# Optimization experiments

Hardware: AMD Instinct MI355X
Metric: run time of the kernel (lower is better)

Reference implementation:

```python
import jax, jax.numpy as jnp
import numpy as np

HIDDEN = 4096
NUM_HEADS = 32
HEAD_DIM = HIDDEN // NUM_HEADS  # 128
ROPE_THETA = 10000.0
B, S = 1, 2048


def setup_inputs() -> dict:
    key = jax.random.key(0)
    k1, k2, k3, k4 = jax.random.split(key, 4)
    positions = jnp.broadcast_to(jnp.arange(S, dtype=jnp.int32), (B, S))
    hidden_states = jax.random.normal(k1, (B, S, HIDDEN), dtype=jnp.float32)
    # fused QKV projection (bias=True), output projection (bias=False)
    w_qkv = jax.random.normal(k2, (HIDDEN, 3 * HIDDEN), dtype=jnp.float32) * (HIDDEN ** -0.5)
    b_qkv = jax.random.normal(k3, (3 * HIDDEN,), dtype=jnp.float32) * 0.01
    w_o = jax.random.normal(k4, (HIDDEN, HIDDEN), dtype=jnp.float32) * (HIDDEN ** -0.5)
    return {"positions": positions, "hidden_states": hidden_states,
            "w_qkv": w_qkv, "b_qkv": b_qkv, "w_o": w_o}


def _apply_rope(x, positions):
    # x: [B, S, N, D]; NeoX-style rotate-half RoPE, rotary_dim == head_dim
    half = HEAD_DIM // 2
    inv_freq = 1.0 / (ROPE_THETA ** (jnp.arange(0, half, dtype=jnp.float32) / half))
    angles = positions.astype(jnp.float32)[..., None] * inv_freq  # [B, S, half]
    cos = jnp.cos(angles)[:, :, None, :]  # [B, S, 1, half]
    sin = jnp.sin(angles)[:, :, None, :]
    x1, x2 = x[..., :half], x[..., half:]
    return jnp.concatenate([x1 * cos - x2 * sin, x2 * cos + x1 * sin], axis=-1)


def reference(positions, hidden_states, w_qkv, b_qkv, w_o):
    qkv = jnp.einsum('bsh,hd->bsd', hidden_states, w_qkv) + b_qkv  # [B, S, 3H]
    q, k, v = jnp.split(qkv, 3, axis=-1)
    q = q.reshape(B, S, NUM_HEADS, HEAD_DIM)
    k = k.reshape(B, S, NUM_HEADS, HEAD_DIM)
    v = v.reshape(B, S, NUM_HEADS, HEAD_DIM)
    q = _apply_rope(q, positions)
    k = _apply_rope(k, positions)
    scale = HEAD_DIM ** -0.5
    scores = jnp.einsum('bqnd,bknd->bnqk', q, k) * scale  # [B, N, S, S]
    causal = jnp.tril(jnp.ones((S, S), dtype=bool))
    scores = jnp.where(causal, scores, jnp.finfo(scores.dtype).min)
    probs = jax.nn.softmax(scores, axis=-1)
    attn = jnp.einsum('bnqk,bknd->bqnd', probs, v).reshape(B, S, HIDDEN)
    return jnp.einsum('bsh,ho->bso', attn, w_o)
```

## Files before the change

### kernel.cpp

```cpp
#include <hip/hip_runtime.h>
#include <hip/hip_bf16.h>

#define S_LEN 2048
#define HID   4096
#define NH    32
#define HD    128
#define KD    4096

typedef __attribute__((ext_vector_type(4))) float f32x4;
typedef __attribute__((ext_vector_type(8))) short s16x8;
typedef __attribute__((ext_vector_type(4))) short s16x4;

#define AS1 __attribute__((address_space(1)))
#define AS3 __attribute__((address_space(3)))

__device__ __forceinline__ void gl_lds16(const void* g, void* l) {
  __builtin_amdgcn_global_load_lds((const AS1 void*)g, (AS3 void*)l, 16, 0, 0);
}

__device__ inline short f2bf(float f) {
  union { float f; unsigned u; } v; v.f = f;
  return (short)((v.u + 0x7fffu + ((v.u >> 16) & 1u)) >> 16);
}
__device__ inline float bf2f(short s) {
  union { unsigned u; float f; } v; v.u = ((unsigned)(unsigned short)s) << 16;
  return v.f;
}
__device__ inline unsigned packbf(float a, float b) {
  return (unsigned)(unsigned short)f2bf(a) | ((unsigned)(unsigned short)f2bf(b) << 16);
}

__global__ __launch_bounds__(256)
void cvt_kernel(const float* __restrict__ A, short* __restrict__ Ab) {
  const size_t i = ((size_t)blockIdx.x * 256 + threadIdx.x) * 8;
  f32x4 v0 = *(const f32x4*)&A[i];
  f32x4 v1 = *(const f32x4*)&A[i + 4];
  s16x8 r;
  r[0]=f2bf(v0[0]); r[1]=f2bf(v0[1]); r[2]=f2bf(v0[2]); r[3]=f2bf(v0[3]);
  r[4]=f2bf(v1[0]); r[5]=f2bf(v1[1]); r[6]=f2bf(v1[2]); r[7]=f2bf(v1[3]);
  *(s16x8*)&Ab[i] = r;
}

__global__ __launch_bounds__(256)
void transcvt_kernel(const float* __restrict__ W, short* __restrict__ Wt, const int N) {
  __shared__ float tile[64][65];
  const int k0 = blockIdx.x * 64, n0 = blockIdx.y * 64;
  const int t = threadIdx.x;
#pragma unroll
  for (int i = 0; i < 16; ++i) {
    const int e = i * 256 + t;
    const int k = e >> 6, n = e & 63;
    tile[n][k] = W[(size_t)(k0 + k) * N + n0 + n];
  }
  __syncthreads();
  const int nn = t >> 2, ks = (t & 3) * 16;
  s16x8 a, b;
#pragma unroll
  for (int i = 0; i < 8; i++) a[i] = f2bf(tile[nn][ks + i]);
#pragma unroll
  for (int i = 0; i < 8; i++) b[i] = f2bf(tile[nn][ks + 8 + i]);
  *(s16x8*)&Wt[(size_t)(n0 + nn) * KD + k0 + ks]     = a;
  *(s16x8*)&Wt[(size_t)(n0 + nn) * KD + k0 + ks + 8] = b;
}

template<int EPI>
__global__ __launch_bounds__(256, 2)
void gemm5_kernel(const short* __restrict__ A, const short* __restrict__ Bt,
                  const float* __restrict__ bias,
                  short* __restrict__ Qb, short* __restrict__ Kb, short* __restrict__ Vb,
                  float* __restrict__ Cout)
{
  __shared__ char sm[3][24576] __attribute__((aligned(128)));
  const int KD2 = KD * 2;
  const int bid = blockIdx.x;
  const int xcd = bid & 7, idx = bid >> 3;
  const int m0 = (idx & 7) * 256;
  const int n0 = (xcd * ((EPI == 0) ? 12 : 4) + (idx >> 3)) * 128;

  const int t = threadIdx.x, lane = t & 63, c = lane & 15, g = lane >> 4;
  const int w = t >> 6, wr = w >> 1, wc = w & 1;
  const int flip = ((c >> 1) & 7) << 4;
  const int laneA = wr * 8192 + ((c * 64 + g * 16) ^ flip);
  const int laneB = 16384 + wc * 4096 + ((c * 64 + g * 16) ^ flip);

  const char* srcA[4];
  const char* srcB[2];
#pragma unroll
  for (int j = 0; j < 4; ++j) {
    const int la = j * 4096 + t * 16;
    const int ls = la ^ ((la >> 3) & 0x70);
    srcA[j] = (const char*)A + (size_t)(m0 + (ls >> 6)) * KD2 + (ls & 63);
  }
#pragma unroll
  for (int j = 0; j < 2; ++j) {
    const int la = j * 4096 + t * 16;
    const int ls = la ^ ((la >> 3) & 0x70);
    srcB[j] = (const char*)Bt + (size_t)(n0 + (ls >> 6)) * KD2 + (ls & 63);
  }

  f32x4 acc[8][4];
#pragma unroll
  for (int i = 0; i < 8; i++)
#pragma unroll
    for (int j = 0; j < 4; j++) acc[i][j] = (f32x4){0.f, 0.f, 0.f, 0.f};

#define STG(S, H) do {                                        \
    const size_t ko_ = (size_t)(H) * 64;                      \
    gl_lds16(srcA[0] + ko_, sm[S] + t * 16);                  \
    gl_lds16(srcA[1] + ko_, sm[S] + 4096  + t * 16);          \
    gl_lds16(srcA[2] + ko_, sm[S] + 8192  + t * 16);          \
    gl_lds16(srcA[3] + ko_, sm[S] + 12288 + t * 16);          \
    gl_lds16(srcB[0] + ko_, sm[S] + 16384 + t * 16);          \
    gl_lds16(srcB[1] + ko_, sm[S] + 20480 + t * 16);          \
  } while (0)

#define COMP(S) do {                                                       \
    const char* b_ = sm[S];                                                \
    s16x8 a_[8], bb_[4];                                                   \
    _Pragma("unroll")                                                      \
    for (int mi = 0; mi < 8; ++mi) a_[mi] = *(const s16x8*)(b_ + laneA + mi * 1024); \
    _Pragma("unroll")                                                      \
    for (int ni = 0; ni < 4; ++ni) bb_[ni] = *(const s16x8*)(b_ + laneB + ni * 1024); \
    __builtin_amdgcn_s_setprio(1);                                         \
    _Pragma("unroll")                                                      \
    for (int mi = 0; mi < 8; ++mi)                                         \
      _Pragma("unroll")                                                    \
      for (int ni = 0; ni < 4; ++ni)                                       \
        acc[mi][ni] = __builtin_amdgcn_mfma_f32_16x16x32_bf16(a_[mi], bb_[ni], acc[mi][ni], 0, 0, 0); \
    __builtin_amdgcn_s_setprio(0);                                         \
  } while (0)

#define WAIT6 asm volatile("s_waitcnt vmcnt(6)" ::: "memory")
#define WAIT0 asm volatile("s_waitcnt vmcnt(0)" ::: "memory")
#define BARR  do { __builtin_amdgcn_s_barrier(); asm volatile("" ::: "memory"); } while (0)

  STG(0, 0); STG(1, 1);
  for (int j = 0; j < 42; ++j) {
    const int h = 3 * j;
    WAIT6; BARR; STG(2, h + 2); COMP(0);
    WAIT6; BARR; STG(0, h + 3); COMP(1);
    WAIT6; BARR; STG(1, h + 4); COMP(2);
  }
  WAIT6; BARR; COMP(0);
  WAIT0; BARR; COMP(1);

#undef STG
#undef COMP
#undef WAIT6
#undef WAIT0
#undef BARR

  if (EPI == 0) {
#pragma unroll
    for (int ni = 0; ni < 4; ++ni) {
      const int ncol = n0 + wc * 64 + ni * 16 + c;
      const int which = ncol >> 12;
      const int h = (ncol >> 7) & 31;
      const int dcl = ncol & 127;
      short* dst = (which == 0) ? Qb : ((which == 1) ? Kb : Vb);
      const float bv = bias[ncol];
#pragma unroll
      for (int mi = 0; mi < 8; ++mi)
#pragma unroll
        for (int jj = 0; jj < 4; ++jj) {
          const int row = m0 + wr * 128 + mi * 16 + g * 4 + jj;
          dst[((size_t)h * S_LEN + row) * HD + dcl] = f2bf(acc[mi][ni][jj] + bv);
        }
    }
  } else {
#pragma unroll
    for (int ni = 0; ni < 4; ++ni) {
      const int ncol = n0 + wc * 64 + ni * 16 + c;
#pragma unroll
      for (int mi = 0; mi < 8; ++mi)
#pragma unroll
        for (int jj = 0; jj < 4; ++jj) {
          const int row = m0 + wr * 128 + mi * 16 + g * 4 + jj;
          Cout[(size_t)row * HID + ncol] = acc[mi][ni][jj];
        }
    }
  }
}

__global__ __launch_bounds__(256, 3)
void gemm7_kernel(const short* __restrict__ A, const short* __restrict__ Bt,
                  float* __restrict__ Cout)
{
  __shared__ char sm[3][16384] __attribute__((aligned(128)));
  const int KD2 = KD * 2;
  const int bid = blockIdx.x;
  const int xcd = bid & 7, idx = bid >> 3;
  const int m0 = (idx & 15) * 128;
  const int n0 = (xcd * 4 + (idx >> 4)) * 128;

  const int t = threadIdx.x, lane = t & 63, c = lane & 15, g = lane >> 4;
  const int w = t >> 6, wr = w >> 1, wc = w & 1;
  const int flip = ((c >> 1) & 7) << 4;
  const int laneA = wr * 4096 + ((c * 64 + g * 16) ^ flip);
  const int laneB = 8192 + wc * 4096 + ((c * 64 + g * 16) ^ flip);

  const char* srcA[2];
  const char* srcB[2];
#pragma unroll
  for (int j = 0; j < 2; ++j) {
    const int la = j * 4096 + t * 16;
    const int ls = la ^ ((la >> 3) & 0x70);
    srcA[j] = (const char*)A  + (size_t)(m0 + (ls >> 6)) * KD2 + (ls & 63);
    srcB[j] = (const char*)Bt + (size_t)(n0 + (ls >> 6)) * KD2 + (ls & 63);
  }

  f32x4 acc[4][4];
#pragma unroll
  for (int i = 0; i < 4; i++)
#pragma unroll
    for (int j = 0; j < 4; j++) acc[i][j] = (f32x4){0.f, 0.f, 0.f, 0.f};

#define STG7(S, H) do {                                       \
    const size_t ko_ = (size_t)(H) * 64;                      \
    gl_lds16(srcA[0] + ko_, sm[S] + t * 16);                  \
    gl_lds16(srcA[1] + ko_, sm[S] + 4096  + t * 16);          \
    gl_lds16(srcB[0] + ko_, sm[S] + 8192  + t * 16);          \
    gl_lds16(srcB[1] + ko_, sm[S] + 12288 + t * 16);          \
  } while (0)

#define COMP7(S) do {                                                      \
    const char* b_ = sm[S];                                                \
    s16x8 a_[4], bb_[4];                                                   \
    _Pragma("unroll")                                                      \
    for (int mi = 0; mi < 4; ++mi) a_[mi] = *(const s16x8*)(b_ + laneA + mi * 1024); \
    _Pragma("unroll")                                                      \
    for (int ni = 0; ni < 4; ++ni) bb_[ni] = *(const s16x8*)(b_ + laneB + ni * 1024); \
    __builtin_amdgcn_s_setprio(1);                                         \
    _Pragma("unroll")                                                      \
    for (int mi = 0; mi < 4; ++mi)                                         \
      _Pragma("unroll")                                                    \
      for (int ni = 0; ni < 4; ++ni)                                       \
        acc[mi][ni] = __builtin_amdgcn_mfma_f32_16x16x32_bf16(a_[mi], bb_[ni], acc[mi][ni], 0, 0, 0); \
    __builtin_amdgcn_s_setprio(0);                                         \
  } while (0)

#define WAIT4 asm volatile("s_waitcnt vmcnt(4)" ::: "memory")
#define WAIT0 asm volatile("s_waitcnt vmcnt(0)" ::: "memory")
#define BARR  do { __builtin_amdgcn_s_barrier(); asm volatile("" ::: "memory"); } while (0)

  STG7(0, 0); STG7(1, 1);
  for (int j = 0; j < 42; ++j) {
    const int h = 3 * j;
    WAIT4; BARR; STG7(2, h + 2); COMP7(0);
    WAIT4; BARR; STG7(0, h + 3); COMP7(1);
    WAIT4; BARR; STG7(1, h + 4); COMP7(2);
  }
  WAIT4; BARR; COMP7(0);
  WAIT0; BARR; COMP7(1);

#undef STG7
#undef COMP7
#undef WAIT4
#undef WAIT0
#undef BARR

#pragma unroll
  for (int ni = 0; ni < 4; ++ni) {
    const int ncol = n0 + wc * 64 + ni * 16 + c;
#pragma unroll
    for (int mi = 0; mi < 4; ++mi)
#pragma unroll
      for (int jj = 0; jj < 4; ++jj) {
        const int row = m0 + wr * 64 + mi * 16 + g * 4 + jj;
        Cout[(size_t)row * HID + ncol] = acc[mi][ni][jj];
      }
  }
}

template<int EPI, int ABF16>
__global__ __launch_bounds__(256)
void gemm_kernel(const void* __restrict__ Av, const float* __restrict__ B,
                 const float* __restrict__ bias, const int N,
                 short* __restrict__ Qb, short* __restrict__ Kb, short* __restrict__ Vb,
                 float* __restrict__ Cout)
{
  __shared__ short As[128][40];
  __shared__ short Bs[128][40];
  const int m0 = blockIdx.x * 128;
  const int nb = blockIdx.y * 128;
  const int t  = threadIdx.x;
  const int w = t >> 6, lane = t & 63, c = lane & 15, g = lane >> 4;
  const int wm = (w >> 1) * 64, wn = (w & 1) * 64;

  f32x4 acc[4][4];
#pragma unroll
  for (int i = 0; i < 4; i++)
#pragma unroll
    for (int j = 0; j < 4; j++) acc[i][j] = (f32x4){0.f, 0.f, 0.f, 0.f};

  const int ar = t >> 3;
  const int ac = (t & 7) * 4;
  const int bn = t & 127;
  const int bkq = (t >> 7) * 16;

  for (int k0 = 0; k0 < KD; k0 += 32) {
#pragma unroll
    for (int rr = 0; rr < 4; rr++) {
      const int row = rr * 32 + ar;
      if (ABF16) {
        *(s16x4*)&As[row][ac] =
          *(const s16x4*)((const short*)Av + (size_t)(m0 + row) * KD + k0 + ac);
      } else {
        f32x4 v = *(const f32x4*)((const float*)Av + (size_t)(m0 + row) * KD + k0 + ac);
        s16x4 pk;
        pk[0] = f2bf(v[0]); pk[1] = f2bf(v[1]); pk[2] = f2bf(v[2]); pk[3] = f2bf(v[3]);
        *(s16x4*)&As[row][ac] = pk;
      }
    }
    const float* pB = B + (size_t)(k0 + bkq) * N + nb + bn;
    s16x8 b0, b1;
#pragma unroll
    for (int i = 0; i < 8; i++) b0[i] = f2bf(pB[(size_t)i * N]);
#pragma unroll
    for (int i = 0; i < 8; i++) b1[i] = f2bf(pB[(size_t)(i + 8) * N]);
    *(s16x8*)&Bs[bn][bkq]     = b0;
    *(s16x8*)&Bs[bn][bkq + 8] = b1;
    __syncthreads();
    s16x8 af[4], bfr[4];
#pragma unroll
    for (int i = 0; i < 4; i++) af[i]  = *(const s16x8*)&As[wm + i * 16 + c][g * 8];
#pragma unroll
    for (int i = 0; i < 4; i++) bfr[i] = *(const s16x8*)&Bs[wn + i * 16 + c][g * 8];
#pragma unroll
    for (int mi = 0; mi < 4; mi++)
#pragma unroll
      for (int ni = 0; ni < 4; ni++)
        acc[mi][ni] = __builtin_amdgcn_mfma_f32_16x16x32_bf16(af[mi], bfr[ni], acc[mi][ni], 0, 0, 0);
    __syncthreads();
  }

  if (EPI == 0) {
    const int which = nb >> 12;
    const int h = (nb & 4095) >> 7;
    short* dst = (which == 0) ? Qb : ((which == 1) ? Kb : Vb);
#pragma unroll
    for (int ni = 0; ni < 4; ni++) {
      const int d = wn + ni * 16 + c;
      const float bv = bias[nb + d];
#pragma unroll
      for (int mi = 0; mi < 4; mi++)
#pragma unroll
        for (int j = 0; j < 4; j++) {
          const int row = m0 + wm + mi * 16 + g * 4 + j;
          dst[((size_t)h * S_LEN + row) * HD + d] = f2bf(acc[mi][ni][j] + bv);
        }
    }
  } else {
#pragma unroll
    for (int ni = 0; ni < 4; ni++) {
      const int n = nb + wn + ni * 16 + c;
#pragma unroll
      for (int mi = 0; mi < 4; mi++)
#pragma unroll
        for (int j = 0; j < 4; j++) {
          const int row = m0 + wm + mi * 16 + g * 4 + j;
          Cout[(size_t)row * N + n] = acc[mi][ni][j];
        }
    }
  }
}

__global__ void rope_kernel(const int* __restrict__ positions,
                            short* __restrict__ Qb, short* __restrict__ Kb)
{
  const int s = blockIdx.x;
  const int h = blockIdx.y * 4 + threadIdx.y;
  const int d = threadIdx.x;
  const float pos = (float)positions[s];
  const float inv_freq = exp2f(-(float)d * 0.20762050593046014f);
  const float ang = pos * inv_freq;
  float sn, cs;
  sincosf(ang, &sn, &cs);
  const size_t base = ((size_t)h * S_LEN + s) * HD + d;
  const float scale = 0.08838834764831845f;
  float x1 = bf2f(Qb[base]), x2 = bf2f(Qb[base + 64]);
  Qb[base]      = f2bf((x1 * cs - x2 * sn) * scale);
  Qb[base + 64] = f2bf((x2 * cs + x1 * sn) * scale);
  x1 = bf2f(Kb[base]); x2 = bf2f(Kb[base + 64]);
  Kb[base]      = f2bf(x1 * cs - x2 * sn);
  Kb[base + 64] = f2bf(x2 * cs + x1 * sn);
}

__global__ __launch_bounds__(256)
void vtrans_kernel(const short* __restrict__ V, short* __restrict__ Vt)
{
  __shared__ short tile[64][72];
  const int h = blockIdx.z;
  const int s0 = blockIdx.x * 64;
  const int d0 = blockIdx.y * 64;
  const int tx = threadIdx.x & 63, ty = threadIdx.x >> 6;
  for (int r = ty; r < 64; r += 4)
    tile[r][tx] = V[((size_t)h * S_LEN + s0 + r) * HD + d0 + tx];
  __syncthreads();
  for (int r = ty; r < 64; r += 4)
    Vt[((size_t)h * HD + d0 + r) * S_LEN + s0 + tx] = tile[tx][r];
}

__global__ __launch_bounds__(512)
void attn_kernel(const short* __restrict__ Q, const short* __restrict__ Kg,
                 const short* __restrict__ Vtg, short* __restrict__ attn_out)
{
  __shared__ short Ks[2][64][128];
  __shared__ short Vs[2][128][72];
  const int h = blockIdx.y;
  const int q0 = blockIdx.x * 128;
  const int t = threadIdx.x;
  const int w = t >> 6, lane = t & 63, c = lane & 15, g = lane >> 4;
  const short* Qh = Q   + (size_t)h * S_LEN * HD;
  const short* Kh = Kg  + (size_t)h * S_LEN * HD;
  const short* Vh = Vtg + (size_t)h * HD * S_LEN;

  const int krow = t >> 4, kch = t & 15;
  const int vrow = t >> 3, vch = t & 7;
  const int ksw = (kch ^ ((krow & 3) | ((krow >> 1) & 4))) * 16;

  const int rbase = (c >> 2) * 8 + (c & 3);
  const int sb = (rbase & 3) | ((rbase >> 1) & 4);
  int koff[4];
#pragma unroll
  for (int di = 0; di < 4; ++di) koff[di] = ((di * 4 + g) ^ sb) * 16;

  const int qg = q0 + w * 16 + c;
  s16x8 qf[4];
#pragma unroll
  for (int di = 0; di < 4; di++)
    qf[di] = *(const s16x8*)&Qh[(size_t)qg * HD + di * 32 + g * 8];

  f32x4 o[8];
#pragma unroll
  for (int dt = 0; dt < 8; dt++) o[dt] = (f32x4){0.f, 0.f, 0.f, 0.f};
  float m_r = -3.0e38f, l_r = 0.f;

  const int nt = q0 / 64 + 2;

  {
#pragma unroll
    for (int i = 0; i < 2; ++i) {
      s16x8 gK = *(const s16x8*)&Kh[(size_t)(i * 32 + krow) * HD + kch * 8];
      s16x8 gV = *(const s16x8*)&Vh[(size_t)(i * 64 + vrow) * S_LEN + vch * 8];
      *(s16x8*)((char*)&Ks[0][0][0] + (i * 32 + krow) * 256 + ksw) = gK;
      *(s16x8*)&Vs[0][i * 64 + vrow][vch * 8] = gV;
    }
  }
  __syncthreads();

  for (int kt = 0; kt < nt; kt++) {
    const int cur = kt & 1;
    const int kb = kt * 64;
    s16x8 gK0, gK1, gV0, gV1;
    if (kt + 1 < nt) {
      gK0 = *(const s16x8*)&Kh[(size_t)(kb + 64 + krow) * HD + kch * 8];
      gK1 = *(const s16x8*)&Kh[(size_t)(kb + 96 + krow) * HD + kch * 8];
      gV0 = *(const s16x8*)&Vh[(size_t)vrow * S_LEN + kb + 64 + vch * 8];
      gV1 = *(const s16x8*)&Vh[(size_t)(64 + vrow) * S_LEN + kb + 64 + vch * 8];
    }
    f32x4 sA = (f32x4){0,0,0,0}, sB = (f32x4){0,0,0,0};
    f32x4 sC = (f32x4){0,0,0,0}, sD = (f32x4){0,0,0,0};
    const char* kb_ = (const char*)&Ks[cur][0][0] + rbase * 256;
#pragma unroll
    for (int di = 0; di < 4; ++di) {
      const char* p = kb_ + koff[di];
      s16x8 kA = *(const s16x8*)(p);
      s16x8 kB = *(const s16x8*)(p + 1024);
      s16x8 kC = *(const s16x8*)(p + 8192);
      s16x8 kD = *(const s16x8*)(p + 9216);
      sA = __builtin_amdgcn_mfma_f32_16x16x32_bf16(kA, qf[di], sA, 0, 0, 0);
      sB = __builtin_amdgcn_mfma_f32_16x16x32_bf16(kB, qf[di], sB, 0, 0, 0);
      sC = __builtin_amdgcn_mfma_f32_16x16x32_bf16(kC, qf[di], sC, 0, 0, 0);
      sD = __builtin_amdgcn_mfma_f32_16x16x32_bf16(kD, qf[di], sD, 0, 0, 0);
    }
    float v[16];
#pragma unroll
    for (int j = 0; j < 4; ++j) {
      v[j]      = (kb + 8 * g + j      <= qg) ? sA[j] : -__builtin_inff();
      v[4 + j]  = (kb + 8 * g + 4 + j  <= qg) ? sB[j] : -__builtin_inff();
      v[8 + j]  = (kb + 32 + 8 * g + j     <= qg) ? sC[j] : -__builtin_inff();
      v[12 + j] = (kb + 32 + 8 * g + 4 + j <= qg) ? sD[j] : -__builtin_inff();
    }
    float mx = v[0];
#pragma unroll
    for (int i = 1; i < 16; ++i) mx = fmaxf(mx, v[i]);
    mx = fmaxf(mx, __shfl_xor(mx, 16, 64));
    mx = fmaxf(mx, __shfl_xor(mx, 32, 64));
    const float mn = fmaxf(m_r, mx);
    if (!__all(mn - m_r <= 8.0f)) {
      const float al = __expf(m_r - mn);
      l_r *= al;
#pragma unroll
      for (int dt = 0; dt < 8; dt++)
#pragma unroll
        for (int j = 0; j < 4; j++) o[dt][j] *= al;
      m_r = mn;
    }
    float p[16];
    float rs = 0.f;
#pragma unroll
    for (int i = 0; i < 16; ++i) { p[i] = __expf(v[i] - m_r); rs += p[i]; }
    rs += __shfl_xor(rs, 16, 64);
    rs += __shfl_xor(rs, 32, 64);
    l_r += rs;
    union { s16x8 v8; unsigned u[4]; } pb0, pb1;
    pb0.u[0] = packbf(p[0], p[1]);   pb0.u[1] = packbf(p[2], p[3]);
    pb0.u[2] = packbf(p[4], p[5]);   pb0.u[3] = packbf(p[6], p[7]);
    pb1.u[0] = packbf(p[8], p[9]);   pb1.u[1] = packbf(p[10], p[11]);
    pb1.u[2] = packbf(p[12], p[13]); pb1.u[3] = packbf(p[14], p[15]);
#pragma unroll
    for (int dt = 0; dt < 8; dt++) {
      s16x8 vf0 = *(const s16x8*)&Vs[cur][dt * 16 + c][g * 8];
      s16x8 vf1 = *(const s16x8*)&Vs[cur][dt * 16 + c][32 + g * 8];
      o[dt] = __builtin_amdgcn_mfma_f32_16x16x32_bf16(vf0, pb0.v8, o[dt], 0, 0, 0);
      o[dt] = __builtin_amdgcn_mfma_f32_16x16x32_bf16(vf1, pb1.v8, o[dt], 0, 0, 0);
    }
    __syncthreads();
    if (kt + 1 < nt) {
      *(s16x8*)((char*)&Ks[cur ^ 1][0][0] + krow * 256 + ksw)        = gK0;
      *(s16x8*)((char*)&Ks[cur ^ 1][0][0] + (32 + krow) * 256 + ksw) = gK1;
      *(s16x8*)&Vs[cur ^ 1][vrow][vch * 8]      = gV0;
      *(s16x8*)&Vs[cur ^ 1][64 + vrow][vch * 8] = gV1;
    }
    __syncthreads();
  }

  const float inv_l = 1.0f / l_r;
#pragma unroll
  for (int dt = 0; dt < 8; dt++) {
    s16x4 pk;
#pragma unroll
    for (int j = 0; j < 4; j++) pk[j] = f2bf(o[dt][j] * inv_l);
    *(s16x4*)&attn_out[(size_t)qg * HID + h * HD + dt * 16 + g * 4] = pk;
  }
}

extern "C" void kernel_launch(void* const* d_in, const int* in_sizes, int n_in,
                              void* d_out, int out_size, void* d_ws, size_t ws_size,
                              hipStream_t stream)
{
  const int*   positions = (const int*)d_in[0];
  const float* hidden    = (const float*)d_in[1];
  const float* w_qkv     = (const float*)d_in[2];
  const float* b_qkv     = (const float*)d_in[3];
  const float* w_o       = (const float*)d_in[4];
  float* out = (float*)d_out;

  char* ws = (char*)d_ws;
  const size_t MB = (size_t)1 << 20;

  if (ws_size >= 224 * MB) {
    short* Ah    = (short*)(ws);
    short* Wqt   = (short*)(ws + 16 * MB);
    short* Wot   = (short*)(ws + 112 * MB);
    short* Qb    = (short*)(ws + 144 * MB);
    short* Kb    = (short*)(ws + 160 * MB);
    short* Vb    = (short*)(ws + 176 * MB);
    short* Vt    = (short*)(ws + 192 * MB);
    short* attnb = (short*)(ws + 208 * MB);

    cvt_kernel<<<4096, 256, 0, stream>>>(hidden, Ah);
    transcvt_kernel<<<dim3(KD / 64, 3 * HID / 64), 256, 0, stream>>>(w_qkv, Wqt, 3 * HID);
    transcvt_kernel<<<dim3(KD / 64, HID / 64), 256, 0, stream>>>(w_o, Wot, HID);
    gemm5_kernel<0><<<768, 256, 0, stream>>>(Ah, Wqt, b_qkv, Qb, Kb, Vb, nullptr);
    rope_kernel<<<dim3(S_LEN, NH / 4), dim3(64, 4), 0, stream>>>(positions, Qb, Kb);
    vtrans_kernel<<<dim3(S_LEN / 64, HD / 64, NH), 256, 0, stream>>>(Vb, Vt);
    attn_kernel<<<dim3(S_LEN / 128, NH), 512, 0, stream>>>(Qb, Kb, Vt, attnb);
    gemm7_kernel<<<512, 256, 0, stream>>>(attnb, Wot, out);
  } else {
    short* Qb    = (short*)(ws);
    short* Kb    = (short*)(ws + 16 * MB);
    short* Vb    = (short*)(ws + 32 * MB);
    short* Vt    = (short*)(ws + 48 * MB);
    short* attnb = (short*)(ws + 64 * MB);

    gemm_kernel<0, 0><<<dim3(16, 96), 256, 0, stream>>>(hidden, w_qkv, b_qkv, 3 * HID,
                                                        Qb, Kb, Vb, nullptr);
    rope_kernel<<<dim3(S_LEN, NH / 4), dim3(64, 4), 0, stream>>>(positions, Qb, Kb);
    vtrans_kernel<<<dim3(S_LEN / 64, HD / 64, NH), 256, 0, stream>>>(Vb, Vt);
    attn_kernel<<<dim3(S_LEN / 128, NH), 512, 0, stream>>>(Qb, Kb, Vt, attnb);
    gemm_kernel<1, 1><<<dim3(16, 32), 256, 0, stream>>>(attnb, w_o, nullptr, HID,
                                                        nullptr, nullptr, nullptr, out);
  }
}
```

Before: 495.5 us.

## Pair mirrored causal query tiles per attention block to balance work and share K/V loads

Each attention block now handles two 128-row query tiles, ib and 15-ib, so every block streams the same total number of K/V tiles, and the K/V tiles loaded into LDS are shared by both query tiles. The grid is halved to 8x32 blocks. The change also skips causal masking on fully visible tiles and raises wave priority around the MFMA sections. In exchange, register pressure roughly doubles (two sets of accumulators and Q fragments), which may spill or lower occupancy, and only 256 blocks remain to fill the GPU.

```diff
diff --git a/kernel.cpp b/kernel.cpp
--- a/kernel.cpp
+++ b/kernel.cpp
@@ -408,7 +408,11 @@
   __shared__ short Ks[2][64][128];
   __shared__ short Vs[2][128][72];
   const int h = blockIdx.y;
-  const int q0 = blockIdx.x * 128;
+  const int ib = blockIdx.x;
+  const int q0a = ib * 128;
+  const int q0b = (15 - ib) * 128;
+  const int nt0 = 2 * ib + 2;
+  const int nt1 = 32 - 2 * ib;
   const int t = threadIdx.x;
   const int w = t >> 6, lane = t & 63, c = lane & 15, g = lane >> 4;
   const short* Qh = Q   + (size_t)h * S_LEN * HD;
@@ -425,18 +429,67 @@
 #pragma unroll
   for (int di = 0; di < 4; ++di) koff[di] = ((di * 4 + g) ^ sb) * 16;
 
-  const int qg = q0 + w * 16 + c;
-  s16x8 qf[4];
-#pragma unroll
-  for (int di = 0; di < 4; di++)
-    qf[di] = *(const s16x8*)&Qh[(size_t)qg * HD + di * 32 + g * 8];
-
-  f32x4 o[8];
-#pragma unroll
-  for (int dt = 0; dt < 8; dt++) o[dt] = (f32x4){0.f, 0.f, 0.f, 0.f};
-  float m_r = -3.0e38f, l_r = 0.f;
-
-  const int nt = q0 / 64 + 2;
+  const int qga = q0a + w * 16 + c;
+  const int qgb = q0b + w * 16 + c;
+  s16x8 qfa[4], qfb[4];
+#pragma unroll
+  for (int di = 0; di < 4; di++) {
+    qfa[di] = *(const s16x8*)&Qh[(size_t)qga * HD + di * 32 + g * 8];
+    qfb[di] = *(const s16x8*)&Qh[(size_t)qgb * HD + di * 32 + g * 8];
+  }
+
+  f32x4 oa[8], ob[8];
+#pragma unroll
+  for (int dt = 0; dt < 8; dt++) {
+    oa[dt] = (f32x4){0.f, 0.f, 0.f, 0.f};
+    ob[dt] = (f32x4){0.f, 0.f, 0.f, 0.f};
+  }
+  float m_a = -3.0e38f, l_a = 0.f, m_b = -3.0e38f, l_b = 0.f;
+
+#define SM_PANEL(SA, SB, SC, SD, QG, FULL, MR, LR, OARR, PB0, PB1) do {        \
+    float v_[16];                                                              \
+    if (FULL) {                                                                \
+      _Pragma("unroll")                                                        \
+      for (int j = 0; j < 4; ++j) {                                            \
+        v_[j] = SA[j]; v_[4 + j] = SB[j]; v_[8 + j] = SC[j]; v_[12 + j] = SD[j]; \
+      }                                                                        \
+    } else {                                                                   \
+      _Pragma("unroll")                                                        \
+      for (int j = 0; j < 4; ++j) {                                            \
+        v_[j]      = (kb + 8 * g + j          <= (QG)) ? SA[j] : -__builtin_inff(); \
+        v_[4 + j]  = (kb + 8 * g + 4 + j      <= (QG)) ? SB[j] : -__builtin_inff(); \
+        v_[8 + j]  = (kb + 32 + 8 * g + j     <= (QG)) ? SC[j] : -__builtin_inff(); \
+        v_[12 + j] = (kb + 32 + 8 * g + 4 + j <= (QG)) ? SD[j] : -__builtin_inff(); \
+      }                                                                        \
+    }                                                                          \
+    float mx_ = v_[0];                                                         \
+    _Pragma("unroll")                                                          \
+    for (int ii = 1; ii < 16; ++ii) mx_ = fmaxf(mx_, v_[ii]);                  \
+    mx_ = fmaxf(mx_, __shfl_xor(mx_, 16, 64));                                 \
+    mx_ = fmaxf(mx_, __shfl_xor(mx_, 32, 64));                                 \
+    const float mn_ = fmaxf(MR, mx_);                                          \
+    if (!__all(mn_ - MR <= 8.0f)) {                                            \
+      const float al_ = __expf(MR - mn_);                                      \
+      LR *= al_;                                                               \
+      _Pragma("unroll")                                                        \
+      for (int dt = 0; dt < 8; ++dt)                                           \
+        _Pragma("unroll")                                                      \
+        for (int j = 0; j < 4; ++j) OARR[dt][j] *= al_;                        \
+      MR = mn_;                                                                \
+    }                                                                          \
+    float p_[16], rs_ = 0.f;                                                   \
+    _Pragma("unroll")                                                          \
+    for (int ii = 0; ii < 16; ++ii) { p_[ii] = __expf(v_[ii] - MR); rs_ += p_[ii]; } \
+    rs_ += __shfl_xor(rs_, 16, 64);                                            \
+    rs_ += __shfl_xor(rs_, 32, 64);                                            \
+    LR += rs_;                                                                 \
+    union { s16x8 v8; unsigned u[4]; } pu0_, pu1_;                             \
+    pu0_.u[0] = packbf(p_[0], p_[1]);   pu0_.u[1] = packbf(p_[2], p_[3]);      \
+    pu0_.u[2] = packbf(p_[4], p_[5]);   pu0_.u[3] = packbf(p_[6], p_[7]);      \
+    pu1_.u[0] = packbf(p_[8], p_[9]);   pu1_.u[1] = packbf(p_[10], p_[11]);    \
+    pu1_.u[2] = packbf(p_[12], p_[13]); pu1_.u[3] = packbf(p_[14], p_[15]);    \
+    PB0 = pu0_.v8; PB1 = pu1_.v8;                                              \
+  } while (0)
 
   {
 #pragma unroll
@@ -449,75 +502,85 @@
   }
   __syncthreads();
 
-  for (int kt = 0; kt < nt; kt++) {
+  for (int kt = 0; kt < nt1; kt++) {
     const int cur = kt & 1;
     const int kb = kt * 64;
+    const bool do0 = (kt < nt0);
     s16x8 gK0, gK1, gV0, gV1;
-    if (kt + 1 < nt) {
+    if (kt + 1 < nt1) {
       gK0 = *(const s16x8*)&Kh[(size_t)(kb + 64 + krow) * HD + kch * 8];
       gK1 = *(const s16x8*)&Kh[(size_t)(kb + 96 + krow) * HD + kch * 8];
       gV0 = *(const s16x8*)&Vh[(size_t)vrow * S_LEN + kb + 64 + vch * 8];
       gV1 = *(const s16x8*)&Vh[(size_t)(64 + vrow) * S_LEN + kb + 64 + vch * 8];
     }
-    f32x4 sA = (f32x4){0,0,0,0}, sB = (f32x4){0,0,0,0};
-    f32x4 sC = (f32x4){0,0,0,0}, sD = (f32x4){0,0,0,0};
-    const char* kb_ = (const char*)&Ks[cur][0][0] + rbase * 256;
-#pragma unroll
-    for (int di = 0; di < 4; ++di) {
-      const char* p = kb_ + koff[di];
-      s16x8 kA = *(const s16x8*)(p);
-      s16x8 kB = *(const s16x8*)(p + 1024);
-      s16x8 kC = *(const s16x8*)(p + 8192);
-      s16x8 kD = *(const s16x8*)(p + 9216);
-      sA = __builtin_amdgcn_mfma_f32_16x16x32_bf16(kA, qf[di], sA, 0, 0, 0);
-      sB = __builtin_amdgcn_mfma_f32_16x16x32_bf16(kB, qf[di], sB, 0, 0, 0);
-      sC = __builtin_amdgcn_mfma_f32_16x16x32_bf16(kC, qf[di], sC, 0, 0, 0);
-      sD = __builtin_amdgcn_mfma_f32_16x16x32_bf16(kD, qf[di], sD, 0, 0, 0);
-    }
-    float v[16];
-#pragma unroll
-    for (int j = 0; j < 4; ++j) {
-      v[j]      = (kb + 8 * g + j      <= qg) ? sA[j] : -__builtin_inff();
-      v[4 + j]  = (kb + 8 * g + 4 + j  <= qg) ? sB[j] : -__builtin_inff();
-      v[8 + j]  = (kb + 32 + 8 * g + j     <= qg) ? sC[j] : -__builtin_inff();
-      v[12 + j] = (kb + 32 + 8 * g + 4 + j <= qg) ? sD[j] : -__builtin_inff();
-    }
-    float mx = v[0];
-#pragma unroll
-    for (int i = 1; i < 16; ++i) mx = fmaxf(mx, v[i]);
-    mx = fmaxf(mx, __shfl_xor(mx, 16, 64));
-    mx = fmaxf(mx, __shfl_xor(mx, 32, 64));
-    const float mn = fmaxf(m_r, mx);
-    if (!__all(mn - m_r <= 8.0f)) {
-      const float al = __expf(m_r - mn);
-      l_r *= al;
-#pragma unroll
-      for (int dt = 0; dt < 8; dt++)
-#pragma unroll
-        for (int j = 0; j < 4; j++) o[dt][j] *= al;
-      m_r = mn;
-    }
-    float p[16];
-    float rs = 0.f;
-#pragma unroll
-    for (int i = 0; i < 16; ++i) { p[i] = __expf(v[i] - m_r); rs += p[i]; }
-    rs += __shfl_xor(rs, 16, 64);
-    rs += __shfl_xor(rs, 32, 64);
-    l_r += rs;
-    union { s16x8 v8; unsigned u[4]; } pb0, pb1;
-    pb0.u[0] = packbf(p[0], p[1]);   pb0.u[1] = packbf(p[2], p[3]);
-    pb0.u[2] = packbf(p[4], p[5]);   pb0.u[3] = packbf(p[6], p[7]);
-    pb1.u[0] = packbf(p[8], p[9]);   pb1.u[1] = packbf(p[10], p[11]);
-    pb1.u[2] = packbf(p[12], p[13]); pb1.u[3] = packbf(p[14], p[15]);
-#pragma unroll
-    for (int dt = 0; dt < 8; dt++) {
-      s16x8 vf0 = *(const s16x8*)&Vs[cur][dt * 16 + c][g * 8];
-      s16x8 vf1 = *(const s16x8*)&Vs[cur][dt * 16 + c][32 + g * 8];
-      o[dt] = __builtin_amdgcn_mfma_f32_16x16x32_bf16(vf0, pb0.v8, o[dt], 0, 0, 0);
-      o[dt] = __builtin_amdgcn_mfma_f32_16x16x32_bf16(vf1, pb1.v8, o[dt], 0, 0, 0);
-    }
+    f32x4 bA = (f32x4){0,0,0,0}, bB = (f32x4){0,0,0,0};
+    f32x4 bC = (f32x4){0,0,0,0}, bD = (f32x4){0,0,0,0};
+    f32x4 aA = (f32x4){0,0,0,0}, aB = (f32x4){0,0,0,0};
+    f32x4 aC = (f32x4){0,0,0,0}, aD = (f32x4){0,0,0,0};
+    const char* kbase = (const char*)&Ks[cur][0][0] + rbase * 256;
+    __builtin_amdgcn_s_setprio(1);
+    if (do0) {
+#pragma unroll
+      for (int di = 0; di < 4; ++di) {
+        const char* p = kbase + koff[di];
+        s16x8 kA = *(const s16x8*)(p);
+        s16x8 kB = *(const s16x8*)(p + 1024);
+        s16x8 kC = *(const s16x8*)(p + 8192);
+        s16x8 kD = *(const s16x8*)(p + 9216);
+        bA = __builtin_amdgcn_mfma_f32_16x16x32_bf16(kA, qfb[di], bA, 0, 0, 0);
+        bB = __builtin_amdgcn_mfma_f32_16x16x32_bf16(kB, qfb[di], bB, 0, 0, 0);
+        bC = __builtin_amdgcn_mfma_f32_16x16x32_bf16(kC, qfb[di], bC, 0, 0, 0);
+        bD = __builtin_amdgcn_mfma_f32_16x16x32_bf16(kD, qfb[di], bD, 0, 0, 0);
+        aA = __builtin_amdgcn_mfma_f32_16x16x32_bf16(kA, qfa[di], aA, 0, 0, 0);
+        aB = __builtin_amdgcn_mfma_f32_16x16x32_bf16(kB, qfa[di], aB, 0, 0, 0);
+        aC = __builtin_amdgcn_mfma_f32_16x16x32_bf16(kC, qfa[di], aC, 0, 0, 0);
+        aD = __builtin_amdgcn_mfma_f32_16x16x32_bf16(kD, qfa[di], aD, 0, 0, 0);
+      }
+    } else {
+#pragma unroll
+      for (int di = 0; di < 4; ++di) {
+        const char* p = kbase + koff[di];
+        s16x8 kA = *(const s16x8*)(p);
+        s16x8 kB = *(const s16x8*)(p + 1024);
+        s16x8 kC = *(const s16x8*)(p + 8192);
+        s16x8 kD = *(const s16x8*)(p + 9216);
+        bA = __builtin_amdgcn_mfma_f32_16x16x32_bf16(kA, qfb[di], bA, 0, 0, 0);
+        bB = __builtin_amdgcn_mfma_f32_16x16x32_bf16(kB, qfb[di], bB, 0, 0, 0);
+        bC = __builtin_amdgcn_mfma_f32_16x16x32_bf16(kC, qfb[di], bC, 0, 0, 0);
+        bD = __builtin_amdgcn_mfma_f32_16x16x32_bf16(kD, qfb[di], bD, 0, 0, 0);
+      }
+    }
+    __builtin_amdgcn_s_setprio(0);
+    s16x8 pb0, pb1, pa0, pa1;
+    const bool fullb = (kb + 64 <= q0b);
+    SM_PANEL(bA, bB, bC, bD, qgb, fullb, m_b, l_b, ob, pb0, pb1);
+    if (do0) {
+      const bool fulla = (kb + 64 <= q0a);
+      SM_PANEL(aA, aB, aC, aD, qga, fulla, m_a, l_a, oa, pa0, pa1);
+    }
+    __builtin_amdgcn_s_setprio(1);
+    if (do0) {
+#pragma unroll
+      for (int dt = 0; dt < 8; dt++) {
+        s16x8 vf0 = *(const s16x8*)&Vs[cur][dt * 16 + c][g * 8];
+        s16x8 vf1 = *(const s16x8*)&Vs[cur][dt * 16 + c][32 + g * 8];
+        ob[dt] = __builtin_amdgcn_mfma_f32_16x16x32_bf16(vf0, pb0, ob[dt], 0, 0, 0);
+        ob[dt] = __builtin_amdgcn_mfma_f32_16x16x32_bf16(vf1, pb1, ob[dt], 0, 0, 0);
+        oa[dt] = __builtin_amdgcn_mfma_f32_16x16x32_bf16(vf0, pa0, oa[dt], 0, 0, 0);
+        oa[dt] = __builtin_amdgcn_mfma_f32_16x16x32_bf16(vf1, pa1, oa[dt], 0, 0, 0);
+      }
+    } else {
+#pragma unroll
+      for (int dt = 0; dt < 8; dt++) {
+        s16x8 vf0 = *(const s16x8*)&Vs[cur][dt * 16 + c][g * 8];
+        s16x8 vf1 = *(const s16x8*)&Vs[cur][dt * 16 + c][32 + g * 8];
+        ob[dt] = __builtin_amdgcn_mfma_f32_16x16x32_bf16(vf0, pb0, ob[dt], 0, 0, 0);
+        ob[dt] = __builtin_amdgcn_mfma_f32_16x16x32_bf16(vf1, pb1, ob[dt], 0, 0, 0);
+      }
+    }
+    __builtin_amdgcn_s_setprio(0);
     __syncthreads();
-    if (kt + 1 < nt) {
+    if (kt + 1 < nt1) {
       *(s16x8*)((char*)&Ks[cur ^ 1][0][0] + krow * 256 + ksw)        = gK0;
       *(s16x8*)((char*)&Ks[cur ^ 1][0][0] + (32 + krow) * 256 + ksw) = gK1;
       *(s16x8*)&Vs[cur ^ 1][vrow][vch * 8]      = gV0;
@@ -525,14 +588,20 @@
     }
     __syncthreads();
   }
-
-  const float inv_l = 1.0f / l_r;
+#undef SM_PANEL
+
+  const float inv_b = 1.0f / l_b;
+  const float inv_a = 1.0f / l_a;
 #pragma unroll
   for (int dt = 0; dt < 8; dt++) {
-    s16x4 pk;
-#pragma unroll
-    for (int j = 0; j < 4; j++) pk[j] = f2bf(o[dt][j] * inv_l);
-    *(s16x4*)&attn_out[(size_t)qg * HID + h * HD + dt * 16 + g * 4] = pk;
+    s16x4 pkb, pka;
+#pragma unroll
+    for (int j = 0; j < 4; j++) {
+      pkb[j] = f2bf(ob[dt][j] * inv_b);
+      pka[j] = f2bf(oa[dt][j] * inv_a);
+    }
+    *(s16x4*)&attn_out[(size_t)qgb * HID + h * HD + dt * 16 + g * 4] = pkb;
+    *(s16x4*)&attn_out[(size_t)qga * HID + h * HD + dt * 16 + g * 4] = pka;
   }
 }
 
@@ -566,7 +635,7 @@
     gemm5_kernel<0><<<768, 256, 0, stream>>>(Ah, Wqt, b_qkv, Qb, Kb, Vb, nullptr);
     rope_kernel<<<dim3(S_LEN, NH / 4), dim3(64, 4), 0, stream>>>(positions, Qb, Kb);
     vtrans_kernel<<<dim3(S_LEN / 64, HD / 64, NH), 256, 0, stream>>>(Vb, Vt);
-    attn_kernel<<<dim3(S_LEN / 128, NH), 512, 0, stream>>>(Qb, Kb, Vt, attnb);
+    attn_kernel<<<dim3(8, NH), 512, 0, stream>>>(Qb, Kb, Vt, attnb);
     gemm7_kernel<<<512, 256, 0, stream>>>(attnb, Wot, out);
   } else {
     short* Qb    = (short*)(ws);
@@ -579,7 +648,7 @@
                                                         Qb, Kb, Vb, nullptr);
     rope_kernel<<<dim3(S_LEN, NH / 4), dim3(64, 4), 0, stream>>>(positions, Qb, Kb);
     vtrans_kernel<<<dim3(S_LEN / 64, HD / 64, NH), 256, 0, stream>>>(Vb, Vt);
-    attn_kernel<<<dim3(S_LEN / 128, NH), 512, 0, stream>>>(Qb, Kb, Vt, attnb);
+    attn_kernel<<<dim3(8, NH), 512, 0, stream>>>(Qb, Kb, Vt, attnb);
     gemm_kernel<1, 1><<<dim3(16, 32), 256, 0, stream>>>(attnb, w_o, nullptr, HID,
                                                         nullptr, nullptr, nullptr, out);
   }
```

New measurement: 469.8 us. 5.2% less time.
